# Kernel tuning notes

Measured on AMD Instinct MI355X. Metric: run time of the kernel, lower is better.

Reference implementation:

```python
import jax, jax.numpy as jnp
import numpy as np
import math

D = 1024
H = 16
HEAD_D = D // H  # 64
T = 2048
B = 4


def setup_inputs() -> dict:
    key = jax.random.key(0)
    k1, k2, k3 = jax.random.split(key, 3)
    x = jax.random.normal(k1, (B, T, D), dtype=jnp.float32)
    # c_attn: Linear(d, d + 2*head_d, bias=False) -> weight applied as x @ W
    w_attn = jax.random.normal(k2, (D, D + 2 * HEAD_D), dtype=jnp.float32) * (1.0 / math.sqrt(D))
    w_proj = jax.random.normal(k3, (D, D), dtype=jnp.float32) * (1.0 / math.sqrt(D))
    return {"x": x, "w_attn": w_attn, "w_proj": w_proj}


def reference(x, w_attn, w_proj):
    Bv, Tv, _ = x.shape
    qkv = x @ w_attn  # [B,T,D+2*head_d]
    q = qkv[..., :D].reshape(Bv, Tv, H, HEAD_D).transpose(0, 2, 1, 3)  # [B,H,T,hd]
    k = qkv[..., D:D + HEAD_D]        # [B,T,hd] single shared KV head
    v = qkv[..., D + HEAD_D:]         # [B,T,hd]
    scale = 1.0 / math.sqrt(HEAD_D)
    # att: [B,H,T,T], shared K broadcast over H query heads
    att = jnp.einsum('bhqd,bkd->bhqk', q, k) * scale
    causal = jnp.tril(jnp.ones((Tv, Tv), dtype=bool))  # [T,T]
    att = jnp.where(causal[None, None, :, :], att, -jnp.inf)
    att = jax.nn.softmax(att, axis=-1)
    y = jnp.einsum('bhqk,bkd->bhqd', att, v)           # [B,H,T,hd]
    y = y.transpose(0, 2, 1, 3).reshape(Bv, Tv, D)     # [B,T,D]
    return y @ w_proj
```

## Files before the change

kernel.cpp:

```cpp
#include <hip/hip_runtime.h>

typedef unsigned short u16;
typedef unsigned int u32;
typedef __attribute__((ext_vector_type(8))) short short8;
typedef __attribute__((ext_vector_type(4))) float f32x4;
typedef __attribute__((ext_vector_type(4))) u16 u16x4;
typedef __attribute__((ext_vector_type(2))) u32 uint2v;
typedef __attribute__((ext_vector_type(4))) u32 u32x4;

__device__ __forceinline__ u16 f2bf(float f) {
  union { float f; unsigned u; } x; x.f = f;
  unsigned r = (x.u + 0x7fffu + ((x.u >> 16) & 1u)) >> 16;
  return (u16)r;
}

__device__ __forceinline__ f32x4 mfma16(short8 a, short8 b, f32x4 c) {
  return __builtin_amdgcn_mfma_f32_16x16x32_bf16(a, b, c, 0, 0, 0);
}

__device__ __forceinline__ void gload16(const u16* g, u16* l) {
  __builtin_amdgcn_global_load_lds((const __attribute__((address_space(1))) void*)g,
                                   (__attribute__((address_space(3))) void*)l, 16, 0, 0);
}

__global__ __launch_bounds__(256) void prep(const float* __restrict__ x,
                                            const float* __restrict__ w_attn,
                                            const float* __restrict__ w_proj,
                                            u16* __restrict__ xb,
                                            u16* __restrict__ wat,
                                            u16* __restrict__ wpt) {
  __shared__ float tile[32][33];
  const int bid = blockIdx.x, tid = threadIdx.x;
  if (bid >= 2176) {
    const int id = bid - 2176;
    const f32x4* src = (const f32x4*)(x + (size_t)id * 4096);
    u16x4* dst = (u16x4*)(xb + (size_t)id * 4096);
#pragma unroll
    for (int c = 0; c < 4; ++c) {
      f32x4 v = src[c * 256 + tid];
      u16x4 o;
#pragma unroll
      for (int j = 0; j < 4; ++j) o[j] = f2bf(v[j]);
      dst[c * 256 + tid] = o;
    }
    return;
  }
  const float* src; u16* dst; int C, bx, by;
  if (bid < 1152) { src = w_attn; dst = wat; C = 1152; bx = bid % 36; by = bid / 36; }
  else { int id = bid - 1152; src = w_proj; dst = wpt; C = 1024; bx = id & 31; by = id >> 5; }
  const int R = 1024;
  const int tx = tid & 31, ty = tid >> 5;
  int c = bx * 32 + tx, r0 = by * 32;
#pragma unroll
  for (int i = 0; i < 32; i += 8)
    tile[ty + i][tx] = src[(size_t)(r0 + ty + i) * C + c];
  __syncthreads();
  int oc = r0 + tx, orow0 = bx * 32;
#pragma unroll
  for (int i = 0; i < 32; i += 8)
    dst[(size_t)(orow0 + ty + i) * R + oc] = f2bf(tile[tx][ty + i]);
}

template <bool C_F32, bool VT>
__global__ __launch_bounds__(256) void gemm_bt(const u16* __restrict__ A,
                                               const u16* __restrict__ Bt,
                                               void* __restrict__ Cp,
                                               u16* __restrict__ vt,
                                               int lda, int ldb, int ldc, int K) {
  __shared__ u16 As[2][128 * 32];
  __shared__ u16 Bs[2][128 * 32];
  const int tid = threadIdx.x;
  const int wid = tid >> 6, lane = tid & 63;
  const int quad = lane >> 4, l15 = lane & 15;
  const int m0 = blockIdx.x * 128, n0 = blockIdx.y * 128;
  const int wm = (wid & 1) * 64, wn = (wid >> 1) * 64;
  const int sr = tid >> 2;
  const int sc = (tid & 3) * 8;

  f32x4 acc[4][4] = {};

  auto stage = [&](int t, int bb) {
    const int k0 = t << 5;
#pragma unroll
    for (int cch = 0; cch < 2; ++cch) {
      const int row = sr + cch * 64;
      gload16(A + (size_t)(m0 + row) * lda + k0 + sc, &As[bb][wid * 512 + cch * 2048]);
      gload16(Bt + (size_t)(n0 + row) * ldb + k0 + sc, &Bs[bb][wid * 512 + cch * 2048]);
    }
  };

  const int nk = K >> 5;
  stage(0, 0);
  for (int t = 0; t < nk; ++t) {
    const int bb = t & 1;
    __syncthreads();
    if (t + 1 < nk) stage(t + 1, bb ^ 1);
    short8 a[4], b[4];
#pragma unroll
    for (int i = 0; i < 4; ++i) a[i] = *(const short8*)&As[bb][(wm + 16 * i + l15) * 32 + quad * 8];
#pragma unroll
    for (int j = 0; j < 4; ++j) b[j] = *(const short8*)&Bs[bb][(wn + 16 * j + l15) * 32 + quad * 8];
#pragma unroll
    for (int i = 0; i < 4; ++i)
#pragma unroll
      for (int j = 0; j < 4; ++j)
        acc[i][j] = mfma16(a[i], b[j], acc[i][j]);
  }

#pragma unroll
  for (int i = 0; i < 4; ++i) {
#pragma unroll
    for (int j = 0; j < 4; ++j) {
      const int mrow = m0 + wm + 16 * i + quad * 4;
      const int ncol = n0 + wn + 16 * j + l15;
#pragma unroll
      for (int r = 0; r < 4; ++r) {
        float v = acc[i][j][r];
        if (C_F32) {
          ((float*)Cp)[(size_t)(mrow + r) * ldc + ncol] = v;
        } else {
          u16 hv = f2bf(v);
          ((u16*)Cp)[(size_t)(mrow + r) * ldc + ncol] = hv;
          if (VT) {
            if (ncol >= 1088) {
              int mg = mrow + r;
              int bb2 = mg >> 11, tt = mg & 2047;
              vt[(size_t)(bb2 * 64 + (ncol - 1088)) * 2048 + tt] = hv;
            }
          }
        }
      }
    }
  }
}

__global__ __launch_bounds__(256) void attn_kernel(const u16* __restrict__ qkv,
                                                   const u16* __restrict__ vt,
                                                   u16* __restrict__ y) {
  const int T = 2048, LD = 1152;
  __shared__ u16 Ks[64 * 68];
  __shared__ u16 Vts[64 * 68];

  const int bid = blockIdx.x;
  const int qt = 15 - (bid >> 6);
  const int bh = bid & 63, b = bh >> 4, h = bh & 15;
  const int q0 = qt * 128;
  const int tid = threadIdx.x, wid = tid >> 6, lane = tid & 63;
  const int quad = lane >> 4, l15 = lane & 15;
  const int wq = wid * 32;
  const u16* qkvb = qkv + (size_t)b * T * LD;
  const u16* vtb = vt + (size_t)b * 64 * 2048;
  const int sr0 = tid >> 3, sc0 = (tid & 7) * 8;
  const int sr1 = sr0 + 32;
  const float c1 = 0.18033688f;
  const float M = 18.0f;
  short8 ones;
#pragma unroll
  for (int j = 0; j < 8; ++j) ones[j] = (short)0x3F80;

  short8 qreg[2][2];
#pragma unroll
  for (int jt = 0; jt < 2; ++jt)
#pragma unroll
    for (int ks = 0; ks < 2; ++ks)
      qreg[jt][ks] = *(const short8*)(qkvb + (size_t)(q0 + wq + 16 * jt + l15) * LD + h * 64 + ks * 32 + quad * 8);

  f32x4 acc[4][2] = {};
  f32x4 accs[2] = {};

  short8 kr0 = *(const short8*)(qkvb + (size_t)sr0 * LD + 1024 + sc0);
  short8 kr1 = *(const short8*)(qkvb + (size_t)sr1 * LD + 1024 + sc0);
  short8 vr0 = *(const short8*)(vtb + (size_t)sr0 * 2048 + sc0);
  short8 vr1 = *(const short8*)(vtb + (size_t)sr1 * 2048 + sc0);

  const int ktmax = 2 * qt + 2;
  for (int kt = 0; kt < ktmax; ++kt) {
    const int kv0 = kt * 64;
    __syncthreads();
    *(short8*)&Ks[sr0 * 68 + sc0] = kr0;
    *(short8*)&Ks[sr1 * 68 + sc0] = kr1;
    *(short8*)&Vts[sr0 * 68 + sc0] = vr0;
    *(short8*)&Vts[sr1 * 68 + sc0] = vr1;
    __syncthreads();
    if (kt + 1 < ktmax) {
      const int nv0 = kv0 + 64;
      kr0 = *(const short8*)(qkvb + (size_t)(nv0 + sr0) * LD + 1024 + sc0);
      kr1 = *(const short8*)(qkvb + (size_t)(nv0 + sr1) * LD + 1024 + sc0);
      vr0 = *(const short8*)(vtb + (size_t)sr0 * 2048 + nv0 + sc0);
      vr1 = *(const short8*)(vtb + (size_t)sr1 * 2048 + nv0 + sc0);
    }
    if (kv0 > q0 + wq + 31) continue;

    f32x4 st[4][2] = {};
#pragma unroll
    for (int ks = 0; ks < 2; ++ks) {
      short8 kf[4];
#pragma unroll
      for (int i = 0; i < 4; ++i) kf[i] = *(const short8*)&Ks[(16 * i + l15) * 68 + ks * 32 + quad * 8];
#pragma unroll
      for (int i = 0; i < 4; ++i)
#pragma unroll
        for (int jt = 0; jt < 2; ++jt)
          st[i][jt] = mfma16(kf[i], qreg[jt][ks], st[i][jt]);
    }

    const bool needMask = (kv0 + 63 > q0 + wq);
    short8 pf[2][2];
#pragma unroll
    for (int jt = 0; jt < 2; ++jt) {
      const int qg = q0 + wq + 16 * jt + l15;
      u32 W[4][2];
#pragma unroll
      for (int i = 0; i < 4; ++i) {
        float p[4];
#pragma unroll
        for (int r = 0; r < 4; ++r) {
          p[r] = __builtin_amdgcn_exp2f(fmaf(st[i][jt][r], c1, -M));
          if (needMask && (kv0 + 16 * i + quad * 4 + r > qg)) p[r] = 0.f;
        }
        asm("v_cvt_pk_bf16_f32 %0, %1, %2" : "=v"(W[i][0]) : "v"(p[0]), "v"(p[1]));
        asm("v_cvt_pk_bf16_f32 %0, %1, %2" : "=v"(W[i][1]) : "v"(p[2]), "v"(p[3]));
      }
#pragma unroll
      for (int ks = 0; ks < 2; ++ks) {
        u32 P0, P1, P2, P3;
        {
          uint2v a = __builtin_amdgcn_permlane32_swap(W[2 * ks][0], W[2 * ks + 1][0], false, false);
          uint2v s = __builtin_amdgcn_permlane16_swap(a[0], a[1], false, false);
          P0 = s[0]; P2 = s[1];
        }
        {
          uint2v a = __builtin_amdgcn_permlane32_swap(W[2 * ks][1], W[2 * ks + 1][1], false, false);
          uint2v s = __builtin_amdgcn_permlane16_swap(a[0], a[1], false, false);
          P1 = s[0]; P3 = s[1];
        }
        union { u32x4 u; short8 s; } cv;
        cv.u = (u32x4){P0, P1, P2, P3};
        pf[jt][ks] = cv.s;
      }
    }

#pragma unroll
    for (int ks = 0; ks < 2; ++ks) {
#pragma unroll
      for (int id = 0; id < 4; ++id) {
        short8 vf = *(const short8*)&Vts[(16 * id + l15) * 68 + ks * 32 + quad * 8];
        acc[id][0] = mfma16(vf, pf[0][ks], acc[id][0]);
        acc[id][1] = mfma16(vf, pf[1][ks], acc[id][1]);
      }
      accs[0] = mfma16(ones, pf[0][ks], accs[0]);
      accs[1] = mfma16(ones, pf[1][ks], accs[1]);
    }
  }

#pragma unroll
  for (int jt = 0; jt < 2; ++jt) {
    const float inv = 1.f / accs[jt][0];
    const int qg = q0 + wq + 16 * jt + l15;
#pragma unroll
    for (int id = 0; id < 4; ++id) {
      u16x4 o;
#pragma unroll
      for (int r = 0; r < 4; ++r) o[r] = f2bf(acc[id][jt][r] * inv);
      *(u16x4*)(y + (size_t)(b * T + qg) * 1024 + h * 64 + 16 * id + quad * 4) = o;
    }
  }
}

extern "C" void kernel_launch(void* const* d_in, const int* in_sizes, int n_in,
                              void* d_out, int out_size, void* d_ws, size_t ws_size,
                              hipStream_t stream) {
  const float* x = (const float*)d_in[0];
  const float* w_attn = (const float*)d_in[1];
  const float* w_proj = (const float*)d_in[2];
  float* out = (float*)d_out;
  char* ws = (char*)d_ws;

  u16* wat = (u16*)ws;
  u16* wpt = (u16*)(ws + 2359296);
  u16* xb  = (u16*)(ws + 4456448);
  u16* qkv = (u16*)(ws + 21233664);
  u16* vt  = (u16*)(ws + 40108032);
  u16* y   = (u16*)(ws + 41156608);

  prep<<<dim3(4224), dim3(256), 0, stream>>>(x, w_attn, w_proj, xb, wat, wpt);
  gemm_bt<false, true><<<dim3(64, 9), 256, 0, stream>>>(xb, wat, qkv, vt, 1024, 1024, 1152, 1024);
  attn_kernel<<<dim3(1024), dim3(256), 0, stream>>>(qkv, vt, y);
  gemm_bt<true, false><<<dim3(64, 8), 256, 0, stream>>>(y, wpt, out, nullptr, 1024, 1024, 1024, 1024);
}
```

Before: 205.7 us.

## Double-buffer K/V tiles via async global-to-LDS loads with XOR swizzle

Replaces register-staged K/V prefetch in the attention kernel with direct global_load_lds writes into double-buffered shared memory. This removes one barrier per iteration and the register round-trip. Shared-memory padding is replaced by an XOR swizzle so that fragment reads avoid bank conflicts. It relies on the barrier waiting for the async LDS loads to finish, and it doubles the LDS footprint.

New measurement: 205.5 us. No clear change (-0.1%).

```diff
diff --git a/kernel.cpp b/kernel.cpp
--- a/kernel.cpp
+++ b/kernel.cpp
@@ -138,8 +138,8 @@
                                                    const u16* __restrict__ vt,
                                                    u16* __restrict__ y) {
   const int T = 2048, LD = 1152;
-  __shared__ u16 Ks[64 * 68];
-  __shared__ u16 Vts[64 * 68];
+  __shared__ u16 Ks[2][64 * 64];
+  __shared__ u16 Vts[2][64 * 64];
 
   const int bid = blockIdx.x;
   const int qt = 15 - (bid >> 6);
@@ -150,8 +150,8 @@
   const int wq = wid * 32;
   const u16* qkvb = qkv + (size_t)b * T * LD;
   const u16* vtb = vt + (size_t)b * 64 * 2048;
-  const int sr0 = tid >> 3, sc0 = (tid & 7) * 8;
-  const int sr1 = sr0 + 32;
+  const int srow = lane >> 3;
+  const int sgx = (lane & 7) ^ srow;
   const float c1 = 0.18033688f;
   const float M = 18.0f;
   short8 ones;
@@ -168,27 +168,23 @@
   f32x4 acc[4][2] = {};
   f32x4 accs[2] = {};
 
-  short8 kr0 = *(const short8*)(qkvb + (size_t)sr0 * LD + 1024 + sc0);
-  short8 kr1 = *(const short8*)(qkvb + (size_t)sr1 * LD + 1024 + sc0);
-  short8 vr0 = *(const short8*)(vtb + (size_t)sr0 * 2048 + sc0);
-  short8 vr1 = *(const short8*)(vtb + (size_t)sr1 * 2048 + sc0);
+  auto stage = [&](int kv0n, int bb) {
+#pragma unroll
+    for (int c = 0; c < 2; ++c) {
+      const int rb = wid * 16 + c * 8;
+      const int row = rb + srow;
+      gload16(qkvb + (size_t)(kv0n + row) * LD + 1024 + sgx * 8, &Ks[bb][rb * 64]);
+      gload16(vtb + (size_t)row * 2048 + kv0n + sgx * 8, &Vts[bb][rb * 64]);
+    }
+  };
 
   const int ktmax = 2 * qt + 2;
+  stage(0, 0);
   for (int kt = 0; kt < ktmax; ++kt) {
     const int kv0 = kt * 64;
+    const int buf = kt & 1;
     __syncthreads();
-    *(short8*)&Ks[sr0 * 68 + sc0] = kr0;
-    *(short8*)&Ks[sr1 * 68 + sc0] = kr1;
-    *(short8*)&Vts[sr0 * 68 + sc0] = vr0;
-    *(short8*)&Vts[sr1 * 68 + sc0] = vr1;
-    __syncthreads();
-    if (kt + 1 < ktmax) {
-      const int nv0 = kv0 + 64;
-      kr0 = *(const short8*)(qkvb + (size_t)(nv0 + sr0) * LD + 1024 + sc0);
-      kr1 = *(const short8*)(qkvb + (size_t)(nv0 + sr1) * LD + 1024 + sc0);
-      vr0 = *(const short8*)(vtb + (size_t)sr0 * 2048 + nv0 + sc0);
-      vr1 = *(const short8*)(vtb + (size_t)sr1 * 2048 + nv0 + sc0);
-    }
+    if (kt + 1 < ktmax) stage(kv0 + 64, buf ^ 1);
     if (kv0 > q0 + wq + 31) continue;
 
     f32x4 st[4][2] = {};
@@ -196,7 +192,8 @@
     for (int ks = 0; ks < 2; ++ks) {
       short8 kf[4];
 #pragma unroll
-      for (int i = 0; i < 4; ++i) kf[i] = *(const short8*)&Ks[(16 * i + l15) * 68 + ks * 32 + quad * 8];
+      for (int i = 0; i < 4; ++i)
+        kf[i] = *(const short8*)&Ks[buf][(16 * i + l15) * 64 + (((ks * 4 + quad) ^ (l15 & 7)) * 8)];
 #pragma unroll
       for (int i = 0; i < 4; ++i)
 #pragma unroll
@@ -244,7 +241,7 @@
     for (int ks = 0; ks < 2; ++ks) {
 #pragma unroll
       for (int id = 0; id < 4; ++id) {
-        short8 vf = *(const short8*)&Vts[(16 * id + l15) * 68 + ks * 32 + quad * 8];
+        short8 vf = *(const short8*)&Vts[buf][(16 * id + l15) * 64 + (((ks * 4 + quad) ^ (l15 & 7)) * 8)];
         acc[id][0] = mfma16(vf, pf[0][ks], acc[id][0]);
         acc[id][1] = mfma16(vf, pf[1][ks], acc[id][1]);
       }
```
